# Performance work log

Hardware: AMD Instinct MI355X
Metric: run time of the kernel (lower is better)

Reference implementation:

```python
import jax, jax.numpy as jnp
import numpy as np

D, N_EXP, N_TOK = 2048, 8, 32768


def setup_inputs() -> dict:
    key = jax.random.key(0)
    k_h, k_eps, k_ww, k_bw, k_wn, k_bn = jax.random.split(key, 6)
    bound = 1.0 / np.sqrt(D)  # nn.Linear default init range
    return {
        "h": jax.random.normal(k_h, (N_TOK, D), dtype=jnp.float32),
        "W_w": jax.random.uniform(k_ww, (D, N_EXP), jnp.float32, -bound, bound),
        "b_w": jax.random.uniform(k_bw, (N_EXP,), jnp.float32, -bound, bound),
        "W_n": jax.random.uniform(k_wn, (D, N_EXP), jnp.float32, -bound, bound),
        "b_n": jax.random.uniform(k_bn, (N_EXP,), jnp.float32, -bound, bound),
        "eps": jax.random.normal(k_eps, (N_TOK, N_EXP), dtype=jnp.float32),
        "top_k": 2,
    }


def reference(h, W_w, b_w, W_n, b_n, eps, top_k):
    # logits = lin_w(h); noise_scale = softplus(lin_noise(h))
    logits = jnp.einsum("td,de->te", h, W_w) + b_w          # [T, E]
    noise = eps * jax.nn.softplus(jnp.einsum("td,de->te", h, W_n) + b_n)
    noisy = logits + noise                                   # [T, E]
    full = jax.nn.softmax(noisy, axis=-1)
    topk_vals, ix = jax.lax.top_k(noisy, top_k)              # [T, k]
    # scatter topk values into -inf tensor == mask non-topk with -inf
    mask = jax.nn.one_hot(ix, noisy.shape[-1], dtype=jnp.bool_).any(axis=-2)  # [T, E]
    sparse = jnp.where(mask, noisy, -jnp.inf)
    return jax.nn.softmax(sparse, axis=-1), ix, full
```

## Files before the change

### kernel.cpp

```cpp
#include <hip/hip_runtime.h>
#include <math.h>

constexpr int D_DIM = 2048;
constexpr int NEXP  = 8;
constexpr int NTOK  = 32768;
constexpr int TT    = 4;
constexpr int KC    = 128;
constexpr int WPB   = 4;

typedef float vf4 __attribute__((ext_vector_type(4)));

__device__ __forceinline__ float softplus_f(float x) {
    return (x > 20.0f) ? x : log1pf(expf(x));
}

__global__ __launch_bounds__(256, 4)
void noisy_topk_router(const float* __restrict__ h,
                       const float* __restrict__ Ww,
                       const float* __restrict__ bw,
                       const float* __restrict__ Wn,
                       const float* __restrict__ bn,
                       const float* __restrict__ eps,
                       float* __restrict__ out_sparse,
                       float* __restrict__ out_ix,
                       float* __restrict__ out_full)
{
    const int lane = threadIdx.x & 63;
    const int wave = threadIdx.x >> 6;
    const int t0   = (blockIdx.x * WPB + wave) * TT;
    const int role = lane & 1;
    const int kg   = lane >> 1;

    float p[TT * 8];
#pragma unroll
    for (int i = 0; i < TT * 8; ++i) p[i] = 0.0f;

    const float* __restrict__ Wp = role ? Wn : Ww;
    const float* hbase = h + (size_t)t0 * D_DIM + 4 * kg;

    vf4 hv[TT];
#pragma unroll
    for (int t = 0; t < TT; ++t)
        hv[t] = __builtin_nontemporal_load((const vf4*)(hbase + (size_t)t * D_DIM));

#pragma unroll 1
    for (int k0 = 0; k0 < D_DIM; k0 += KC) {
        const vf4* wp = (const vf4*)(Wp + (size_t)(k0 + 4 * kg) * NEXP);
        vf4 w0 = wp[0], w1 = wp[1], w2 = wp[2], w3 = wp[3],
            w4 = wp[4], w5 = wp[5], w6 = wp[6], w7 = wp[7];

        vf4 hvn[TT];
        if (k0 + KC < D_DIM) {
#pragma unroll
            for (int t = 0; t < TT; ++t)
                hvn[t] = __builtin_nontemporal_load(
                    (const vf4*)(hbase + (size_t)t * D_DIM + (k0 + KC)));
        }

        const float w[32] = {w0[0], w0[1], w0[2], w0[3], w1[0], w1[1], w1[2], w1[3],
                             w2[0], w2[1], w2[2], w2[3], w3[0], w3[1], w3[2], w3[3],
                             w4[0], w4[1], w4[2], w4[3], w5[0], w5[1], w5[2], w5[3],
                             w6[0], w6[1], w6[2], w6[3], w7[0], w7[1], w7[2], w7[3]};

#pragma unroll
        for (int t = 0; t < TT; ++t) {
#pragma unroll
            for (int d = 0; d < 4; ++d) {
                const float x = hv[t][d];
#pragma unroll
                for (int o = 0; o < 8; ++o)
                    p[t * 8 + o] = fmaf(x, w[d * 8 + o], p[t * 8 + o]);
            }
        }

#pragma unroll
        for (int t = 0; t < TT; ++t) hv[t] = hvn[t];
    }

#pragma unroll
    for (int s = 0; s < 5; ++s) {
        const int m = 2 << s;
        const bool hi = (lane & m) != 0;
        const int n = 32 >> (s + 1);
#pragma unroll
        for (int j = 0; j < n; ++j) {
            float a  = p[2 * j];
            float b  = p[2 * j + 1];
            float ta = __shfl_xor(a, m, 64);
            float tb = __shfl_xor(b, m, 64);
            p[j] = hi ? (b + tb) : (a + ta);
        }
    }

    const int  o         = (lane >> 1) & 7;
    const bool noiseLane = (role != 0);
    const int  tok       = t0 + (lane >> 4);
    const float bias     = noiseLane ? bn[o] : bw[o];

    const float val = p[0] + bias;
    const float sp  = softplus_f(val);
    const float spN = __shfl_xor(sp, 1, 64);
    const float ev  = eps[(size_t)tok * NEXP + o];
    const float noisy = val + ev * spN;

    float v0 = noisy; int i0 = o;
#pragma unroll
    for (int m = 2; m <= 8; m <<= 1) {
        float ov = __shfl_xor(v0, m, 64);
        int   oi = __shfl_xor(i0, m, 64);
        bool take = (ov > v0) || (ov == v0 && oi < i0);
        v0 = take ? ov : v0;
        i0 = take ? oi : i0;
    }
    float v1 = (o == i0) ? -INFINITY : noisy; int i1 = o;
#pragma unroll
    for (int m = 2; m <= 8; m <<= 1) {
        float ov = __shfl_xor(v1, m, 64);
        int   oi = __shfl_xor(i1, m, 64);
        bool take = (ov > v1) || (ov == v1 && oi < i1);
        v1 = take ? ov : v1;
        i1 = take ? oi : i1;
    }
    const float ex = expf(noisy - v0);
    float ssum = ex;
#pragma unroll
    for (int m = 2; m <= 8; m <<= 1) ssum += __shfl_xor(ssum, m, 64);
    const float fullv = ex / ssum;
    const float dd  = expf(v1 - v0);
    const float den = 1.0f + dd;
    const float sparsev = (o == i0) ? (1.0f / den)
                        : (o == i1) ? (dd / den) : 0.0f;

    if (!noiseLane) {
        out_sparse[(size_t)tok * NEXP + o] = sparsev;
        out_full  [(size_t)tok * NEXP + o] = fullv;
        if (o == 0) {
            out_ix[(size_t)tok * 2]     = (float)i0;
            out_ix[(size_t)tok * 2 + 1] = (float)i1;
        }
    }
}

extern "C" void kernel_launch(void* const* d_in, const int* in_sizes, int n_in,
                              void* d_out, int out_size, void* d_ws, size_t ws_size,
                              hipStream_t stream) {
    const float* h   = (const float*)d_in[0];
    const float* Ww  = (const float*)d_in[1];
    const float* bw  = (const float*)d_in[2];
    const float* Wn  = (const float*)d_in[3];
    const float* bn  = (const float*)d_in[4];
    const float* eps = (const float*)d_in[5];

    float* out_sparse = (float*)d_out;
    float* out_ix     = out_sparse + (size_t)NTOK * NEXP;
    float* out_full   = out_ix + (size_t)NTOK * 2;

    const int grid = NTOK / (TT * WPB);
    noisy_topk_router<<<grid, 256, 0, stream>>>(h, Ww, bw, Wn, bn, eps,
                                                out_sparse, out_ix, out_full);
}
```

Baseline: 432.4 us.

## Stage router weight chunks through double-buffered LDS shared by block waves

Weight chunks for both projections are now loaded cooperatively by the whole block into a double-buffered, padded shared-memory tile. Each wave then reads its 32 weights per lane from LDS instead of issuing eight vector global loads per chunk. This cuts redundant global/L2 traffic for the small weight matrices across the four waves. In exchange it adds a block-wide barrier per chunk and LDS read traffic, and it drops the nontemporal hint on the h loads. The memory-bound h stream dominates, so the gain is uncertain.

```diff
diff --git a/kernel.cpp b/kernel.cpp
--- a/kernel.cpp
+++ b/kernel.cpp
@@ -6,7 +6,12 @@
 constexpr int NTOK  = 32768;
 constexpr int TT    = 4;
 constexpr int KC    = 128;
+constexpr int NCH   = D_DIM / KC;
 constexpr int WPB   = 4;
+
+constexpr int KGSTR = 33;
+constexpr int MSTR  = 32 * KGSTR;
+constexpr int BSTR  = 2 * MSTR;
 
 typedef float vf4 __attribute__((ext_vector_type(4)));
 
@@ -25,56 +30,85 @@
                        float* __restrict__ out_ix,
                        float* __restrict__ out_full)
 {
-    const int lane = threadIdx.x & 63;
-    const int wave = threadIdx.x >> 6;
+    __shared__ float sW[2 * BSTR];
+
+    const int tid  = threadIdx.x;
+    const int lane = tid & 63;
+    const int wave = tid >> 6;
     const int t0   = (blockIdx.x * WPB + wave) * TT;
     const int role = lane & 1;
     const int kg   = lane >> 1;
+
+    const int s_kg   = tid >> 3;
+    const int s_slot = tid & 7;
+    const int s_dst0 = 0 * MSTR + (s_kg & 31) * KGSTR + s_slot * 4;
+    const int s_dst1 = 1 * MSTR + (s_kg & 31) * KGSTR + s_slot * 4;
+    const int s_src  = (tid & 255) * 4;
 
     float p[TT * 8];
 #pragma unroll
     for (int i = 0; i < TT * 8; ++i) p[i] = 0.0f;
 
-    const float* __restrict__ Wp = role ? Wn : Ww;
     const float* hbase = h + (size_t)t0 * D_DIM + 4 * kg;
 
+    {
+        vf4 a = *(const vf4*)(Ww + s_src);
+        vf4 b = *(const vf4*)(Wn + s_src);
+#pragma unroll
+        for (int i = 0; i < 4; ++i) sW[s_dst0 + i] = a[i];
+#pragma unroll
+        for (int i = 0; i < 4; ++i) sW[s_dst1 + i] = b[i];
+    }
     vf4 hv[TT];
 #pragma unroll
     for (int t = 0; t < TT; ++t)
-        hv[t] = __builtin_nontemporal_load((const vf4*)(hbase + (size_t)t * D_DIM));
+        hv[t] = *(const vf4*)(hbase + (size_t)t * D_DIM);
+    __syncthreads();
 
 #pragma unroll 1
-    for (int k0 = 0; k0 < D_DIM; k0 += KC) {
-        const vf4* wp = (const vf4*)(Wp + (size_t)(k0 + 4 * kg) * NEXP);
-        vf4 w0 = wp[0], w1 = wp[1], w2 = wp[2], w3 = wp[3],
-            w4 = wp[4], w5 = wp[5], w6 = wp[6], w7 = wp[7];
+    for (int c = 0; c < NCH; ++c) {
+        const int cur = c & 1;
+        const bool more = (c + 1 < NCH);
 
+        vf4 wa, wb;
+        if (more) {
+            const int src = (c + 1) * (KC * NEXP) + s_src;
+            wa = *(const vf4*)(Ww + src);
+            wb = *(const vf4*)(Wn + src);
+        }
         vf4 hvn[TT];
-        if (k0 + KC < D_DIM) {
+        if (more) {
 #pragma unroll
             for (int t = 0; t < TT; ++t)
-                hvn[t] = __builtin_nontemporal_load(
-                    (const vf4*)(hbase + (size_t)t * D_DIM + (k0 + KC)));
+                hvn[t] = *(const vf4*)(hbase + (size_t)t * D_DIM + (c + 1) * KC);
         }
 
-        const float w[32] = {w0[0], w0[1], w0[2], w0[3], w1[0], w1[1], w1[2], w1[3],
-                             w2[0], w2[1], w2[2], w2[3], w3[0], w3[1], w3[2], w3[3],
-                             w4[0], w4[1], w4[2], w4[3], w5[0], w5[1], w5[2], w5[3],
-                             w6[0], w6[1], w6[2], w6[3], w7[0], w7[1], w7[2], w7[3]};
+        const int rbase = cur * BSTR + role * MSTR + kg * KGSTR;
+        float w[32];
+#pragma unroll
+        for (int j = 0; j < 32; ++j) w[j] = sW[rbase + j];
 
 #pragma unroll
         for (int t = 0; t < TT; ++t) {
 #pragma unroll
-            for (int d = 0; d < 4; ++d) {
-                const float x = hv[t][d];
+            for (int r = 0; r < 4; ++r) {
+                const float x = hv[t][r];
 #pragma unroll
                 for (int o = 0; o < 8; ++o)
-                    p[t * 8 + o] = fmaf(x, w[d * 8 + o], p[t * 8 + o]);
+                    p[t * 8 + o] = fmaf(x, w[r * 8 + o], p[t * 8 + o]);
             }
         }
 
+        if (more) {
+            const int obase = (cur ^ 1) * BSTR;
 #pragma unroll
-        for (int t = 0; t < TT; ++t) hv[t] = hvn[t];
+            for (int i = 0; i < 4; ++i) sW[obase + s_dst0 + i] = wa[i];
+#pragma unroll
+            for (int i = 0; i < 4; ++i) sW[obase + s_dst1 + i] = wb[i];
+#pragma unroll
+            for (int t = 0; t < TT; ++t) hv[t] = hvn[t];
+        }
+        __syncthreads();
     }
 
 #pragma unroll
```

New measurement: 371.3 us. 14.1% less time.
